# Kernel optimization log

Measured on AMD Instinct MI355X. Metric: run time of the kernel, lower is better.

The kernel has to match this reference:

```python
import jax, jax.numpy as jnp
import numpy as np

DT = 1.0 / 24.0
NEARZERO = 1e-5
LENF = 72
T_STEPS, N_GRID, N_OUT = 1440, 8000, 32

PHY_NAMES = ['parBETA','parFC','parK0','parK1','parK2','parLP','parPERC','parUZL','parTT',
             'parCFMAX','parCFR','parCWH','parBETAET','parC','parRT','parAC','parF0','parFMIN','parALPHA']
PHY_BOUNDS = {'parBETA':(1.0,6.0),'parFC':(50.0,1000.0),'parK0':(0.05,0.9),'parK1':(0.01,0.5),
              'parK2':(0.001,0.2),'parLP':(0.2,1.0),'parPERC':(0.0,10.0),'parUZL':(0.0,100.0),
              'parTT':(-2.5,2.5),'parCFMAX':(0.5,10.0),'parCFR':(0.0,0.1),'parCWH':(0.0,0.2),
              'parBETAET':(0.3,5.0),'parC':(0.0,1.0),'parRT':(0.0,20.0),'parAC':(0.0,2500.0),
              'parF0':(120.0,2880.0),'parFMIN':(0.0,1.0),'parALPHA':(0.5,5.0)}
DISTR_NAMES = ['rout_a','rout_b','rout_tau']
DISTR_BOUNDS = {'rout_a':(0.0,5.0),'rout_b':(0.0,12.0),'rout_tau':(0.0,48.0)}


def _descale(raw, names, bounds):
    # raw in [0,1] -> physical range lb + raw*(ub-lb); each entry is [n_grid]
    return {n: bounds[n][0] + raw[:, i] * (bounds[n][1] - bounds[n][0]) for i, n in enumerate(names)}


def setup_inputs() -> dict:
    key = jax.random.key(0)
    ks = jax.random.split(key, 7)
    u = jax.random.uniform(ks[0], (T_STEPS, N_GRID, 3), dtype=jnp.float32)
    # prcp [0,2) mm/h, tmean [-10,20) C, pet [0,0.3) mm/h
    x_phy = jnp.stack([u[..., 0] * 2.0, u[..., 1] * 30.0 - 10.0, u[..., 2] * 0.3], axis=-1)
    ac_all = jax.random.uniform(ks[1], (N_GRID,), dtype=jnp.float32) * 2000.0        # drainage area km^2
    elev_all = jax.random.uniform(ks[2], (N_GRID,), dtype=jnp.float32) * 3000.0     # elevation m
    outlet_topo = (jax.random.uniform(ks[3], (N_OUT, N_GRID)) < 0.1).astype(jnp.float32)
    areas = jax.random.uniform(ks[4], (N_GRID,), dtype=jnp.float32) * 50.0 + 1.0    # basin area km^2
    params1 = jax.random.uniform(ks[5], (N_GRID, 19), dtype=jnp.float32)            # static phy params
    params2 = jax.random.uniform(ks[6], (N_GRID, 3), dtype=jnp.float32)             # distr routing params
    return {'x_phy': x_phy, 'ac_all': ac_all, 'elev_all': elev_all,
            'outlet_topo': outlet_topo, 'areas': areas, 'params1': params1, 'params2': params2}


def _hbv(x_phy, ac_all, elev_all, outlet_topo, areas, params1, params2):
    p = _descale(params1, PHY_NAMES, PHY_BOUNDS)
    d = _descale(params2, DISTR_NAMES, DISTR_BOUNDS)
    n = x_phy.shape[1]
    init = tuple(jnp.full((n,), 1e-3, x_phy.dtype) for _ in range(5))  # SNOWPACK, MELTWATER, SM, SUZ, SLZ
    # HBV2.0 max hourly infiltration rate, decaying with drainage area (parF0 in mm/day)
    fmax = DT * p['parF0'] * (p['parFMIN'] + (1.0 - p['parFMIN'])
                              * jnp.exp(-(ac_all / (p['parAC'] + 1.0)) ** (1.0 / p['parALPHA'])))

    def step(carry, xt):
        SP, MW, SM, SUZ, SLZ = carry
        P, Tm, PET = xt[:, 0], xt[:, 1], xt[:, 2]
        rain = jnp.where(Tm >= p['parTT'], P, 0.0)
        snow = P - rain
        SP = SP + snow
        melt = jnp.minimum(jnp.maximum(p['parCFMAX'] * DT * (Tm - p['parTT']), 0.0), SP)
        MW = MW + melt; SP = SP - melt
        refr = jnp.minimum(jnp.maximum(p['parCFR'] * p['parCFMAX'] * DT * (p['parTT'] - Tm), 0.0), MW)
        SP = SP + refr; MW = MW - refr
        tosoil = jnp.maximum(MW - p['parCWH'] * SP, 0.0)
        MW = MW - tosoil
        win = rain + tosoil
        infil = jnp.minimum(win, fmax)
        qie = win - infil                                  # infiltration-excess overland flow
        sw = jnp.clip((SM / p['parFC']) ** p['parBETA'], 0.0, 1.0)
        rech = infil * sw
        SM = SM + infil - rech
        excess = jnp.maximum(SM - p['parFC'], 0.0); SM = SM - excess
        cap = jnp.minimum(SLZ, p['parC'] * SLZ * (1.0 - jnp.minimum(SM / p['parFC'], 1.0)))
        SM = SM + cap; SLZ = SLZ - cap                      # capillary rise
        ef = jnp.clip((SM / (p['parLP'] * p['parFC'])) ** p['parBETAET'], 0.0, 1.0)
        et = jnp.minimum(PET * ef, SM)
        SM = jnp.maximum(SM - et, NEARZERO)
        SUZ = SUZ + rech + excess
        perc = jnp.minimum(SUZ, p['parPERC'] * DT); SUZ = SUZ - perc
        q0 = p['parK0'] * DT * jnp.maximum(SUZ - p['parUZL'], 0.0); SUZ = SUZ - q0
        q1 = p['parK1'] * DT * SUZ; SUZ = SUZ - q1
        SLZ = SLZ + perc
        q2 = p['parK2'] * DT * SLZ; SLZ = SLZ - q2
        return (SP, MW, SM, SUZ, SLZ), qie + q0 + q1 + q2

    _, Q = jax.lax.scan(step, init, x_phy)                 # Q: [T, n_grid] grid runoff mm/h

    # Distributed gamma unit hydrograph with per-grid lag (rout_tau + parRT), length LENF hours
    lag = d['rout_tau'] + p['parRT']                       # [n_grid]
    a = jnp.maximum(d['rout_a'], 0.01)
    b = jnp.maximum(d['rout_b'], 0.01)
    tt = jnp.arange(0.5, LENF, 1.0, dtype=x_phy.dtype)     # [LENF]
    s = tt[None, :] - lag[:, None]                          # [n_grid, LENF]
    logw = (a[:, None] - 1.0) * jnp.log(jnp.maximum(s, 1e-6)) - jnp.maximum(s, 1e-6) / b[:, None]
    w = jnp.where(s > 0.0, jnp.exp(logw), 0.0)
    w = w / (jnp.sum(w, axis=1, keepdims=True) + 1e-8)      # normalized per-grid UH [n_grid, LENF]

    # Causal per-grid (depthwise) convolution: routed[t,n] = sum_k w[n,k] * Q[t-k,n]
    lhs = Q.T[None]                                         # [1, n_grid, T]
    rhs = w[:, ::-1][:, None, :]                            # [n_grid, 1, LENF] (flip -> correlation == conv)
    routed = jax.lax.conv_general_dilated(lhs, rhs, (1,), [(LENF - 1, 0)],
                                          feature_group_count=lhs.shape[1])[0].T  # [T, n_grid]
    # Area-weighted aggregation of grid runoff to outlets
    return jnp.einsum('tn,on,n->to', routed, outlet_topo, areas)  # [T, n_out]


def reference(x_phy, ac_all, elev_all, outlet_topo, areas, params1, params2):
    return _hbv(x_phy, ac_all, elev_all, outlet_topo, areas, params1, params2)
```

## Files before the change

### kernel.cpp

```cpp
#include <hip/hip_runtime.h>

#define NG 8000
#define NG3 24000
#define TS 1440
#define NOUT 32
#define LENFT 72
#define DTC (1.0f/24.0f)
#define NEARZEROC 1e-5f

__device__ __forceinline__ float fexp2(float x) {
  float r; asm("v_exp_f32 %0, %1" : "=v"(r) : "v"(x)); return r;
}
__device__ __forceinline__ float flog2(float x) {
  float r; asm("v_log_f32 %0, %1" : "=v"(r) : "v"(x)); return r;
}

typedef const void __attribute__((address_space(1))) gas_void;
typedef void __attribute__((address_space(3)))       las_void;

__global__ __launch_bounds__(256) void precompute_kernel(
    const float* __restrict__ p1, const float* __restrict__ p2,
    const float* __restrict__ ac_all,
    float* __restrict__ Cst,
    float* __restrict__ W)
{
  int n = blockIdx.x * 256 + threadIdx.x;
  if (n >= NG) return;
  const float* r = p1 + n * 19;
  float BETA   = 1.0f   + r[0]  * 5.0f;
  float FC     = 50.0f  + r[1]  * 950.0f;
  float K0     = 0.05f  + r[2]  * 0.85f;
  float K1     = 0.01f  + r[3]  * 0.49f;
  float K2     = 0.001f + r[4]  * 0.199f;
  float LP     = 0.2f   + r[5]  * 0.8f;
  float PERC   =          r[6]  * 10.0f;
  float UZL    =          r[7]  * 100.0f;
  float TT     = -2.5f  + r[8]  * 5.0f;
  float CFMAX  = 0.5f   + r[9]  * 9.5f;
  float CFR    =          r[10] * 0.1f;
  float CWH    =          r[11] * 0.2f;
  float BETAET = 0.3f   + r[12] * 4.7f;
  float Cpar   =          r[13];
  float RT     =          r[14] * 20.0f;
  float AC     =          r[15] * 2500.0f;
  float F0     = 120.0f + r[16] * 2760.0f;
  float FMIN   =          r[17];
  float ALPHA  = 0.5f   + r[18] * 4.5f;

  float ac  = ac_all[n];
  float fmx = DTC * F0 * (FMIN + (1.0f - FMIN) * expf(-powf(ac / (AC + 1.0f), 1.0f / ALPHA)));

  Cst[ 0*NG+n] = TT;            Cst[ 1*NG+n] = CFMAX * DTC;
  Cst[ 2*NG+n] = CFR*CFMAX*DTC; Cst[ 3*NG+n] = CWH;
  Cst[ 4*NG+n] = fmx;           Cst[ 5*NG+n] = 1.0f / FC;
  Cst[ 6*NG+n] = BETA;          Cst[ 7*NG+n] = FC;
  Cst[ 8*NG+n] = Cpar;          Cst[ 9*NG+n] = 1.0f / (LP * FC);
  Cst[10*NG+n] = BETAET;        Cst[11*NG+n] = PERC * DTC;
  Cst[12*NG+n] = K0 * DTC;      Cst[13*NG+n] = UZL;
  Cst[14*NG+n] = K1 * DTC;      Cst[15*NG+n] = K2 * DTC;

  float a   = fmaxf(p2[n*3+0] * 5.0f,  0.01f);
  float b   = fmaxf(p2[n*3+1] * 12.0f, 0.01f);
  float lag = p2[n*3+2] * 48.0f + RT;
  float am1 = a - 1.0f, invb = 1.0f / b;
  float sum = 0.0f;
  for (int k = 0; k < LENFT; k++) {
    float s  = (k + 0.5f) - lag;
    float sm = fmaxf(s, 1e-6f);
    float wv = (s > 0.0f) ? expf(am1 * logf(sm) - sm * invb) : 0.0f;
    sum += wv;
  }
  float inv = 1.0f / (sum + 1e-8f);
  for (int k = 0; k < LENFT; k++) {
    float s  = (k + 0.5f) - lag;
    float sm = fmaxf(s, 1e-6f);
    float wv = (s > 0.0f) ? expf(am1 * logf(sm) - sm * invb) : 0.0f;
    W[k*NG + n] = wv * inv;
  }
}

struct HbvConst {
  float TT, CFMAXDT, CFRDT, CWH, FMX, IFC, BETA, FC, C, ILF, BETAET,
        PERCDT, K0DT, UZL, K1DT, K2DT;
};

__device__ __forceinline__ void load_const(const float* __restrict__ Cst,
                                           int n, HbvConst& c) {
  c.TT    =Cst[ 0*NG+n]; c.CFMAXDT=Cst[ 1*NG+n]; c.CFRDT =Cst[ 2*NG+n];
  c.CWH   =Cst[ 3*NG+n]; c.FMX    =Cst[ 4*NG+n]; c.IFC   =Cst[ 5*NG+n];
  c.BETA  =Cst[ 6*NG+n]; c.FC     =Cst[ 7*NG+n]; c.C     =Cst[ 8*NG+n];
  c.ILF   =Cst[ 9*NG+n]; c.BETAET =Cst[10*NG+n]; c.PERCDT=Cst[11*NG+n];
  c.K0DT  =Cst[12*NG+n]; c.UZL    =Cst[13*NG+n]; c.K1DT  =Cst[14*NG+n];
  c.K2DT  =Cst[15*NG+n];
}

__device__ __forceinline__ float hbv_step(float P, float Tm, float PET,
    const HbvConst& c, float& SP, float& MW, float& SM, float& SUZ, float& SLZ)
{
  bool  w    = Tm >= c.TT;
  float dT   = Tm - c.TT;
  float rain = w ? P : 0.0f;
  SP += P - rain;
  float k  = w ? c.CFMAXDT : c.CFRDT;
  float tr = __builtin_amdgcn_fmed3f(k * dT, -MW, SP);
  MW += tr; SP -= tr;
  float tosoil = fmaxf(MW - c.CWH * SP, 0.0f);
  MW -= tosoil;
  float win   = rain + tosoil;
  float infil = fminf(win, c.FMX);
  float qie   = win - infil;
  float sw    = fminf(fexp2(c.BETA * flog2(SM * c.IFC)), 1.0f);
  float rech  = infil * sw;
  SM += infil - rech;
  float excess = fmaxf(SM - c.FC, 0.0f);
  SM -= excess;
  float u   = fmaxf(1.0f - SM * c.IFC, 0.0f);
  float cap = c.C * SLZ * u;
  SM += cap; SLZ -= cap;
  float ef = fminf(fexp2(c.BETAET * flog2(SM * c.ILF)), 1.0f);
  SM = fmaxf(SM - PET * ef, NEARZEROC);
  SUZ += rech + excess;
  float perc = fminf(SUZ, c.PERCDT);
  SUZ -= perc;
  float q0 = c.K0DT * fmaxf(SUZ - c.UZL, 0.0f);
  SUZ -= q0;
  float q1 = c.K1DT * SUZ;
  SUZ -= q1;
  SLZ += perc;
  float q2 = c.K2DT * SLZ;
  SLZ -= q2;
  return qie + q0 + q1 + q2;
}

#define LOADU8(A, T0)                                                         \
  { _Pragma("unroll")                                                         \
    for (int i_ = 0; i_ < 8; i_++) {                                          \
      const float* b_ = x + (size_t)((T0) + i_) * NG3;                        \
      A[i_] = *reinterpret_cast<const float3*>(b_ + 3 * n);                   \
    } }

__global__ __launch_bounds__(64, 1) void scan_kernel(
    const float* __restrict__ x, const float* __restrict__ Cst,
    float* __restrict__ Q)
{
  int n = blockIdx.x * 64 + threadIdx.x;
  HbvConst c; load_const(Cst, n, c);
  float SP=1e-3f, MW=1e-3f, SM=1e-3f, SUZ=1e-3f, SLZ=1e-3f;

  float3 bufA[8], bufB[8];
  LOADU8(bufA, 0);
  for (int tb = 0; tb < TS; tb += 16) {
    LOADU8(bufB, tb + 8);
    #pragma unroll
    for (int i = 0; i < 8; i++) {
      float* qb = Q + (size_t)(tb + i) * NG;
      qb[n] = hbv_step(bufA[i].x, bufA[i].y, bufA[i].z, c, SP, MW, SM, SUZ, SLZ);
    }
    if (tb + 16 < TS) LOADU8(bufA, tb + 16);
    #pragma unroll
    for (int i = 0; i < 8; i++) {
      float* qb = Q + (size_t)(tb + 8 + i) * NG;
      qb[n] = hbv_step(bufB[i].x, bufB[i].y, bufB[i].z, c, SP, MW, SM, SUZ, SLZ);
    }
  }
}

#define TTILE 48
#define NTILES_T 30
#define NSPLIT 25
#define SUBS 5
#define QROWS (TTILE + 71)
#define NWG (NTILES_T * NSPLIT)

__global__ __launch_bounds__(256, 2) void route_kernel(
    const float* __restrict__ Q, const float* __restrict__ W,
    const float* __restrict__ topo, const float* __restrict__ areas,
    float* __restrict__ Par)
{
  __shared__ float Qs[QROWS][64];
  __shared__ float Ws[LENFT][64];
  __shared__ float Rs[TTILE][68];

  int bid  = blockIdx.x;
  int xcd  = bid & 7, pos = bid >> 3;
  const int q = NWG / 8, r = NWG % 8;
  int wgid = ((xcd < r) ? xcd * (q + 1) : r * (q + 1) + (xcd - r) * q) + pos;
  int tile  = wgid % NTILES_T;
  int split = wgid / NTILES_T;
  int t0    = tile * TTILE;
  int tid   = threadIdx.x;
  int wid   = tid >> 6, lane = tid & 63;

  int nn = tid & 63;
  int tc = wid * 12;
  int oe = tid & 31;
  int te = (tid >> 5) * 6;

  auto stage = [&](int sub) {
    int n0 = (split * SUBS + sub) * 64;
    for (int rr = wid; rr < QROWS; rr += 4) {
      int t = t0 - 71 + rr;
      if (t >= 0)
        __builtin_amdgcn_global_load_lds(
            (gas_void*)(Q + (size_t)t * NG + n0 + lane),
            (las_void*)(&Qs[rr][0]), 4, 0, 0);
      else
        Qs[rr][lane] = 0.0f;
    }
    for (int k = wid; k < LENFT; k += 4)
      __builtin_amdgcn_global_load_lds(
          (gas_void*)(W + (size_t)k * NG + n0 + lane),
          (las_void*)(&Ws[k][0]), 4, 0, 0);
  };

  float acc_out[6] = {0.f, 0.f, 0.f, 0.f, 0.f, 0.f};

  stage(0);
  for (int sub = 0; sub < SUBS; sub++) {
    int n0 = (split * SUBS + sub) * 64;

    float4 Greg[16];
    #pragma unroll
    for (int g4 = 0; g4 < 16; g4++) {
      float4 tv = *reinterpret_cast<const float4*>(&topo[oe * NG + n0 + g4 * 4]);
      float4 av = *reinterpret_cast<const float4*>(&areas[n0 + g4 * 4]);
      Greg[g4] = make_float4(tv.x * av.x, tv.y * av.y, tv.z * av.z, tv.w * av.w);
    }

    __syncthreads();

    float acc[12];
    float qwin[12];
    #pragma unroll
    for (int i = 0; i < 12; i++) { acc[i] = 0.0f; qwin[i] = Qs[tc + i][nn]; }
    #pragma unroll
    for (int kk = 0; kk < LENFT; kk++) {
      float w = Ws[71 - kk][nn];
      #pragma unroll
      for (int i = 0; i < 12; i++) acc[i] += w * qwin[i];
      #pragma unroll
      for (int i = 0; i < 11; i++) qwin[i] = qwin[i + 1];
      if (kk < 71) qwin[11] = Qs[tc + 12 + kk][nn];
    }
    #pragma unroll
    for (int i = 0; i < 12; i++) Rs[tc + i][nn] = acc[i];
    __syncthreads();

    if (sub + 1 < SUBS) stage(sub + 1);

    #pragma unroll
    for (int g4 = 0; g4 < 16; g4++) {
      float4 g = Greg[g4];
      #pragma unroll
      for (int p = 0; p < 6; p++) {
        float4 rv = *reinterpret_cast<const float4*>(&Rs[te + p][g4 * 4]);
        acc_out[p] += rv.x * g.x + rv.y * g.y + rv.z * g.z + rv.w * g.w;
      }
    }
  }

  #pragma unroll
  for (int p = 0; p < 6; p++) {
    int tg = t0 + te + p;
    Par[(split * TS + tg) * NOUT + oe] = acc_out[p];
  }
}

__global__ __launch_bounds__(256) void reduce_kernel(
    const float* __restrict__ Par, float* __restrict__ out)
{
  int i = blockIdx.x * 256 + threadIdx.x;
  if (i < TS * NOUT) {
    float s = 0.0f;
    #pragma unroll
    for (int sp = 0; sp < NSPLIT; sp++) s += Par[sp * (TS * NOUT) + i];
    out[i] = s;
  }
}

extern "C" void kernel_launch(void* const* d_in, const int* in_sizes, int n_in,
                              void* d_out, int out_size, void* d_ws, size_t ws_size,
                              hipStream_t stream)
{
  const float* x_phy  = (const float*)d_in[0];
  const float* ac_all = (const float*)d_in[1];
  const float* topo   = (const float*)d_in[3];
  const float* areas  = (const float*)d_in[4];
  const float* p1     = (const float*)d_in[5];
  const float* p2     = (const float*)d_in[6];
  float* out = (float*)d_out;

  char* ws = (char*)d_ws;
  float* Q   = (float*)(ws);
  float* W   = (float*)(ws + 46080000);
  float* Cst = (float*)(ws + 46080000 + 2304000);
  float* Par = (float*)(ws + 46080000 + 2304000 + 512000);

  hipLaunchKernelGGL(precompute_kernel, dim3(32), dim3(256), 0, stream,
                     p1, p2, ac_all, Cst, W);
  hipLaunchKernelGGL(scan_kernel, dim3(NG / 64), dim3(64), 0, stream,
                     x_phy, Cst, Q);
  hipLaunchKernelGGL(route_kernel, dim3(NWG), dim3(256), 0, stream,
                     Q, W, topo, areas, Par);
  hipLaunchKernelGGL(reduce_kernel, dim3((TS * NOUT + 255) / 256), dim3(256), 0, stream,
                     Par, out);
}
```

Before: 296.6 us.

## Software-pipeline HBV scan by splitting snow and soil stages across time blocks

Splits the per-timestep HBV update into a snow/infiltration stage and a soil/groundwater stage. The snow stage for the next 8-step block now runs interleaved with the soil stage of the current block, with loads rescheduled to match. The aim is more independent instructions in this latency-bound serial scan, which runs with very low occupancy. The cost is more live registers for the staged arrays, plus one redundant snow pass on stale data in the final iteration.

Result: slower. 408.0 us (+37.6%).

```diff
diff --git a/kernel.cpp b/kernel.cpp
--- a/kernel.cpp
+++ b/kernel.cpp
@@ -94,44 +94,6 @@
   c.K2DT  =Cst[15*NG+n];
 }
 
-__device__ __forceinline__ float hbv_step(float P, float Tm, float PET,
-    const HbvConst& c, float& SP, float& MW, float& SM, float& SUZ, float& SLZ)
-{
-  bool  w    = Tm >= c.TT;
-  float dT   = Tm - c.TT;
-  float rain = w ? P : 0.0f;
-  SP += P - rain;
-  float k  = w ? c.CFMAXDT : c.CFRDT;
-  float tr = __builtin_amdgcn_fmed3f(k * dT, -MW, SP);
-  MW += tr; SP -= tr;
-  float tosoil = fmaxf(MW - c.CWH * SP, 0.0f);
-  MW -= tosoil;
-  float win   = rain + tosoil;
-  float infil = fminf(win, c.FMX);
-  float qie   = win - infil;
-  float sw    = fminf(fexp2(c.BETA * flog2(SM * c.IFC)), 1.0f);
-  float rech  = infil * sw;
-  SM += infil - rech;
-  float excess = fmaxf(SM - c.FC, 0.0f);
-  SM -= excess;
-  float u   = fmaxf(1.0f - SM * c.IFC, 0.0f);
-  float cap = c.C * SLZ * u;
-  SM += cap; SLZ -= cap;
-  float ef = fminf(fexp2(c.BETAET * flog2(SM * c.ILF)), 1.0f);
-  SM = fmaxf(SM - PET * ef, NEARZEROC);
-  SUZ += rech + excess;
-  float perc = fminf(SUZ, c.PERCDT);
-  SUZ -= perc;
-  float q0 = c.K0DT * fmaxf(SUZ - c.UZL, 0.0f);
-  SUZ -= q0;
-  float q1 = c.K1DT * SUZ;
-  SUZ -= q1;
-  SLZ += perc;
-  float q2 = c.K2DT * SLZ;
-  SLZ -= q2;
-  return qie + q0 + q1 + q2;
-}
-
 #define LOADU8(A, T0)                                                         \
   { _Pragma("unroll")                                                         \
     for (int i_ = 0; i_ < 8; i_++) {                                          \
@@ -147,21 +109,66 @@
   HbvConst c; load_const(Cst, n, c);
   float SP=1e-3f, MW=1e-3f, SM=1e-3f, SUZ=1e-3f, SLZ=1e-3f;
 
+  auto snow8 = [&](const float3* buf, float* inf, float* qie, float* pet) {
+    #pragma unroll
+    for (int i = 0; i < 8; i++) {
+      float P = buf[i].x, Tm = buf[i].y;
+      bool  w    = Tm >= c.TT;
+      float dT   = Tm - c.TT;
+      float rain = w ? P : 0.0f;
+      SP += P - rain;
+      float k  = w ? c.CFMAXDT : c.CFRDT;
+      float tr = __builtin_amdgcn_fmed3f(k * dT, -MW, SP);
+      MW += tr; SP -= tr;
+      float tos = fmaxf(MW - c.CWH * SP, 0.0f);
+      MW -= tos;
+      float win = rain + tos;
+      float nf  = fminf(win, c.FMX);
+      inf[i] = nf; qie[i] = win - nf; pet[i] = buf[i].z;
+    }
+  };
+  auto soil8 = [&](const float* inf, const float* qie, const float* pet, int tb) {
+    #pragma unroll
+    for (int i = 0; i < 8; i++) {
+      float nf   = inf[i];
+      float sw   = fminf(fexp2(c.BETA * flog2(SM * c.IFC)), 1.0f);
+      float rech = nf * sw;
+      SM += nf - rech;
+      float exc = fmaxf(SM - c.FC, 0.0f);
+      SM -= exc;
+      float u   = fmaxf(1.0f - SM * c.IFC, 0.0f);
+      float cap = c.C * SLZ * u;
+      SM += cap; SLZ -= cap;
+      float ef = fminf(fexp2(c.BETAET * flog2(SM * c.ILF)), 1.0f);
+      SM = fmaxf(SM - pet[i] * ef, NEARZEROC);
+      SUZ += rech + exc;
+      float perc = fminf(SUZ, c.PERCDT);
+      SUZ -= perc;
+      float q0 = c.K0DT * fmaxf(SUZ - c.UZL, 0.0f);
+      SUZ -= q0;
+      float q1 = c.K1DT * SUZ;
+      SUZ -= q1;
+      SLZ += perc;
+      float q2 = c.K2DT * SLZ;
+      SLZ -= q2;
+      (Q + (size_t)(tb + i) * NG)[n] = qie[i] + q0 + q1 + q2;
+    }
+  };
+
   float3 bufA[8], bufB[8];
+  float infA[8], qieA[8], petA[8], infB[8], qieB[8], petB[8];
+
   LOADU8(bufA, 0);
+  snow8(bufA, infA, qieA, petA);
+  LOADU8(bufB, 8);
+
   for (int tb = 0; tb < TS; tb += 16) {
-    LOADU8(bufB, tb + 8);
-    #pragma unroll
-    for (int i = 0; i < 8; i++) {
-      float* qb = Q + (size_t)(tb + i) * NG;
-      qb[n] = hbv_step(bufA[i].x, bufA[i].y, bufA[i].z, c, SP, MW, SM, SUZ, SLZ);
-    }
     if (tb + 16 < TS) LOADU8(bufA, tb + 16);
-    #pragma unroll
-    for (int i = 0; i < 8; i++) {
-      float* qb = Q + (size_t)(tb + 8 + i) * NG;
-      qb[n] = hbv_step(bufB[i].x, bufB[i].y, bufB[i].z, c, SP, MW, SM, SUZ, SLZ);
-    }
+    snow8(bufB, infB, qieB, petB);
+    soil8(infA, qieA, petA, tb);
+    if (tb + 24 < TS) LOADU8(bufB, tb + 24);
+    snow8(bufA, infA, qieA, petA);
+    soil8(infB, qieB, petB, tb + 8);
   }
 }
 
```

## Process two grid cells per thread in HBV scan using packed float2 math

Applied to the files above, without the earlier changes.

The scan kernel now gives each thread two adjacent grid cells and holds the state and constants as 2-wide float vectors, so the compiler can emit packed FP32 ops (v_pk_fma/mul/add) on CDNA. Inputs are loaded as three float2 per timestep and Q is stored as float2, which widens the memory accesses. The trade-off is that the thread count is halved from 8000 to 4000 (63 wavefronts), which lowers latency hiding for the serial recurrence. The exp/log and med3 operations are still scalar.

Result: slower. 399.5 us (+34.7%).

```diff
diff --git a/kernel.cpp b/kernel.cpp
--- a/kernel.cpp
+++ b/kernel.cpp
@@ -1,6 +1,7 @@
 #include <hip/hip_runtime.h>
 
 #define NG 8000
+#define NHALF 4000
 #define NG3 24000
 #define TS 1440
 #define NOUT 32
@@ -17,6 +18,7 @@
 
 typedef const void __attribute__((address_space(1))) gas_void;
 typedef void __attribute__((address_space(3)))       las_void;
+typedef float v2f __attribute__((ext_vector_type(2)));
 
 __global__ __launch_bounds__(256) void precompute_kernel(
     const float* __restrict__ p1, const float* __restrict__ p2,
@@ -79,89 +81,109 @@
   }
 }
 
-struct HbvConst {
-  float TT, CFMAXDT, CFRDT, CWH, FMX, IFC, BETA, FC, C, ILF, BETAET,
-        PERCDT, K0DT, UZL, K1DT, K2DT;
+struct HbvConst2 {
+  v2f TT, CFMAXDT, CFRDT, CWH, FMX, IFC, BETA, FC, C, ILF, BETAET,
+      PERCDT, K0DT, UZL, K1DT, K2DT;
 };
 
-__device__ __forceinline__ void load_const(const float* __restrict__ Cst,
-                                           int n, HbvConst& c) {
-  c.TT    =Cst[ 0*NG+n]; c.CFMAXDT=Cst[ 1*NG+n]; c.CFRDT =Cst[ 2*NG+n];
-  c.CWH   =Cst[ 3*NG+n]; c.FMX    =Cst[ 4*NG+n]; c.IFC   =Cst[ 5*NG+n];
-  c.BETA  =Cst[ 6*NG+n]; c.FC     =Cst[ 7*NG+n]; c.C     =Cst[ 8*NG+n];
-  c.ILF   =Cst[ 9*NG+n]; c.BETAET =Cst[10*NG+n]; c.PERCDT=Cst[11*NG+n];
-  c.K0DT  =Cst[12*NG+n]; c.UZL    =Cst[13*NG+n]; c.K1DT  =Cst[14*NG+n];
-  c.K2DT  =Cst[15*NG+n];
-}
-
-__device__ __forceinline__ float hbv_step(float P, float Tm, float PET,
-    const HbvConst& c, float& SP, float& MW, float& SM, float& SUZ, float& SLZ)
-{
-  bool  w    = Tm >= c.TT;
-  float dT   = Tm - c.TT;
-  float rain = w ? P : 0.0f;
+__device__ __forceinline__ v2f ldc2(const float* __restrict__ Cst, int j, int i2) {
+  return *reinterpret_cast<const v2f*>(Cst + j * NG + i2);
+}
+
+__device__ __forceinline__ v2f hbv_step2p(v2f P, v2f Tm, v2f PET,
+    const HbvConst2& c, v2f& SP, v2f& MW, v2f& SM, v2f& SUZ, v2f& SLZ)
+{
+  const v2f vzero = 0.0f, vone = 1.0f, veps = NEARZEROC;
+  v2f rain, k;
+  rain.x = (Tm.x >= c.TT.x) ? P.x : 0.0f;
+  rain.y = (Tm.y >= c.TT.y) ? P.y : 0.0f;
+  k.x    = (Tm.x >= c.TT.x) ? c.CFMAXDT.x : c.CFRDT.x;
+  k.y    = (Tm.y >= c.TT.y) ? c.CFMAXDT.y : c.CFRDT.y;
+  v2f dT = Tm - c.TT;
   SP += P - rain;
-  float k  = w ? c.CFMAXDT : c.CFRDT;
-  float tr = __builtin_amdgcn_fmed3f(k * dT, -MW, SP);
+  v2f kd = k * dT;
+  v2f tr;
+  tr.x = __builtin_amdgcn_fmed3f(kd.x, -MW.x, SP.x);
+  tr.y = __builtin_amdgcn_fmed3f(kd.y, -MW.y, SP.y);
   MW += tr; SP -= tr;
-  float tosoil = fmaxf(MW - c.CWH * SP, 0.0f);
+  v2f tosoil = __builtin_elementwise_max(MW - c.CWH * SP, vzero);
   MW -= tosoil;
-  float win   = rain + tosoil;
-  float infil = fminf(win, c.FMX);
-  float qie   = win - infil;
-  float sw    = fminf(fexp2(c.BETA * flog2(SM * c.IFC)), 1.0f);
-  float rech  = infil * sw;
+  v2f win   = rain + tosoil;
+  v2f infil = __builtin_elementwise_min(win, c.FMX);
+  v2f qie   = win - infil;
+  v2f lg, sw;
+  lg.x = flog2(SM.x * c.IFC.x);  lg.y = flog2(SM.y * c.IFC.y);
+  sw.x = fexp2(c.BETA.x * lg.x); sw.y = fexp2(c.BETA.y * lg.y);
+  sw = __builtin_elementwise_min(sw, vone);
+  v2f rech = infil * sw;
   SM += infil - rech;
-  float excess = fmaxf(SM - c.FC, 0.0f);
+  v2f excess = __builtin_elementwise_max(SM - c.FC, vzero);
   SM -= excess;
-  float u   = fmaxf(1.0f - SM * c.IFC, 0.0f);
-  float cap = c.C * SLZ * u;
+  v2f u   = __builtin_elementwise_max(vone - SM * c.IFC, vzero);
+  v2f cap = c.C * SLZ * u;
   SM += cap; SLZ -= cap;
-  float ef = fminf(fexp2(c.BETAET * flog2(SM * c.ILF)), 1.0f);
-  SM = fmaxf(SM - PET * ef, NEARZEROC);
+  v2f lg2, ef;
+  lg2.x = flog2(SM.x * c.ILF.x);    lg2.y = flog2(SM.y * c.ILF.y);
+  ef.x  = fexp2(c.BETAET.x * lg2.x); ef.y = fexp2(c.BETAET.y * lg2.y);
+  ef = __builtin_elementwise_min(ef, vone);
+  SM = __builtin_elementwise_max(SM - PET * ef, veps);
   SUZ += rech + excess;
-  float perc = fminf(SUZ, c.PERCDT);
+  v2f perc = __builtin_elementwise_min(SUZ, c.PERCDT);
   SUZ -= perc;
-  float q0 = c.K0DT * fmaxf(SUZ - c.UZL, 0.0f);
+  v2f q0 = c.K0DT * __builtin_elementwise_max(SUZ - c.UZL, vzero);
   SUZ -= q0;
-  float q1 = c.K1DT * SUZ;
+  v2f q1 = c.K1DT * SUZ;
   SUZ -= q1;
   SLZ += perc;
-  float q2 = c.K2DT * SLZ;
+  v2f q2 = c.K2DT * SLZ;
   SLZ -= q2;
   return qie + q0 + q1 + q2;
 }
 
-#define LOADU8(A, T0)                                                         \
+#define LOADP8(A, T0)                                                         \
   { _Pragma("unroll")                                                         \
-    for (int i_ = 0; i_ < 8; i_++) {                                          \
-      const float* b_ = x + (size_t)((T0) + i_) * NG3;                        \
-      A[i_] = *reinterpret_cast<const float3*>(b_ + 3 * n);                   \
+    for (int k_ = 0; k_ < 8; k_++) {                                          \
+      const float* b_ = xp + (size_t)((T0) + k_) * NG3;                       \
+      A[k_][0] = *reinterpret_cast<const v2f*>(b_);                           \
+      A[k_][1] = *reinterpret_cast<const v2f*>(b_ + 2);                       \
+      A[k_][2] = *reinterpret_cast<const v2f*>(b_ + 4);                       \
     } }
+
+#define STEPP(A, k_, t_)                                                      \
+  { v2f P_  = {A[k_][0].x, A[k_][1].y};                                       \
+    v2f Tm_ = {A[k_][0].y, A[k_][2].x};                                       \
+    v2f E_  = {A[k_][1].x, A[k_][2].y};                                       \
+    v2f q_  = hbv_step2p(P_, Tm_, E_, c, SP, MW, SM, SUZ, SLZ);               \
+    *reinterpret_cast<v2f*>(Q + (size_t)(t_) * NG + i2) = q_; }
 
 __global__ __launch_bounds__(64, 1) void scan_kernel(
     const float* __restrict__ x, const float* __restrict__ Cst,
     float* __restrict__ Q)
 {
-  int n = blockIdx.x * 64 + threadIdx.x;
-  HbvConst c; load_const(Cst, n, c);
-  float SP=1e-3f, MW=1e-3f, SM=1e-3f, SUZ=1e-3f, SLZ=1e-3f;
-
-  float3 bufA[8], bufB[8];
-  LOADU8(bufA, 0);
+  int i = blockIdx.x * 64 + threadIdx.x;
+  if (i >= NHALF) return;
+  int i2 = 2 * i;
+
+  HbvConst2 c;
+  c.TT    =ldc2(Cst, 0,i2); c.CFMAXDT=ldc2(Cst, 1,i2); c.CFRDT =ldc2(Cst, 2,i2);
+  c.CWH   =ldc2(Cst, 3,i2); c.FMX    =ldc2(Cst, 4,i2); c.IFC   =ldc2(Cst, 5,i2);
+  c.BETA  =ldc2(Cst, 6,i2); c.FC     =ldc2(Cst, 7,i2); c.C     =ldc2(Cst, 8,i2);
+  c.ILF   =ldc2(Cst, 9,i2); c.BETAET =ldc2(Cst,10,i2); c.PERCDT=ldc2(Cst,11,i2);
+  c.K0DT  =ldc2(Cst,12,i2); c.UZL    =ldc2(Cst,13,i2); c.K1DT  =ldc2(Cst,14,i2);
+  c.K2DT  =ldc2(Cst,15,i2);
+
+  v2f SP = 1e-3f, MW = 1e-3f, SM = 1e-3f, SUZ = 1e-3f, SLZ = 1e-3f;
+  const float* xp = x + (size_t)6 * i;
+
+  v2f bufA[8][3], bufB[8][3];
+  LOADP8(bufA, 0);
   for (int tb = 0; tb < TS; tb += 16) {
-    LOADU8(bufB, tb + 8);
-    #pragma unroll
-    for (int i = 0; i < 8; i++) {
-      float* qb = Q + (size_t)(tb + i) * NG;
-      qb[n] = hbv_step(bufA[i].x, bufA[i].y, bufA[i].z, c, SP, MW, SM, SUZ, SLZ);
-    }
-    if (tb + 16 < TS) LOADU8(bufA, tb + 16);
-    #pragma unroll
-    for (int i = 0; i < 8; i++) {
-      float* qb = Q + (size_t)(tb + 8 + i) * NG;
-      qb[n] = hbv_step(bufB[i].x, bufB[i].y, bufB[i].z, c, SP, MW, SM, SUZ, SLZ);
-    }
+    LOADP8(bufB, tb + 8);
+    #pragma unroll
+    for (int kk = 0; kk < 8; kk++) STEPP(bufA, kk, tb + kk);
+    if (tb + 16 < TS) LOADP8(bufA, tb + 16);
+    #pragma unroll
+    for (int kk = 0; kk < 8; kk++) STEPP(bufB, kk, tb + 8 + kk);
   }
 }
 
@@ -298,7 +320,7 @@
 
   hipLaunchKernelGGL(precompute_kernel, dim3(32), dim3(256), 0, stream,
                      p1, p2, ac_all, Cst, W);
-  hipLaunchKernelGGL(scan_kernel, dim3(NG / 64), dim3(64), 0, stream,
+  hipLaunchKernelGGL(scan_kernel, dim3((NHALF + 63) / 64), dim3(64), 0, stream,
                      x_phy, Cst, Q);
   hipLaunchKernelGGL(route_kernel, dim3(NWG), dim3(256), 0, stream,
                      Q, W, topo, areas, Par);
```

## Fuse scan and routing into a cooperative persistent kernel with progress flags

Applied to the files above, without the earlier changes.

Combines the sequential HBV time scan and the convolution routing into one cooperative launch. 32 high-priority blocks run the scan and bump an atomic progress counter after each 288-step chunk. The remaining persistent blocks spin-wait until the Q rows for their time tile are written, then route, so routing overlaps the scan. The cost is a big change in scan parallelism (256-thread blocks on only 32 CUs instead of 125 small blocks) plus spin-wait overhead. Deadlock is avoided only by the cooperative launch guarantee and a timeout.

Result: slower. 795.8 us (+168.3%).

```diff
diff --git a/kernel.cpp b/kernel.cpp
--- a/kernel.cpp
+++ b/kernel.cpp
@@ -22,8 +22,10 @@
     const float* __restrict__ p1, const float* __restrict__ p2,
     const float* __restrict__ ac_all,
     float* __restrict__ Cst,
-    float* __restrict__ W)
-{
+    float* __restrict__ W,
+    int* __restrict__ prog)
+{
+  if (blockIdx.x == 0 && threadIdx.x == 0) prog[0] = 0;
   int n = blockIdx.x * 256 + threadIdx.x;
   if (n >= NG) return;
   const float* r = p1 + n * 19;
@@ -139,32 +141,6 @@
       A[i_] = *reinterpret_cast<const float3*>(b_ + 3 * n);                   \
     } }
 
-__global__ __launch_bounds__(64, 1) void scan_kernel(
-    const float* __restrict__ x, const float* __restrict__ Cst,
-    float* __restrict__ Q)
-{
-  int n = blockIdx.x * 64 + threadIdx.x;
-  HbvConst c; load_const(Cst, n, c);
-  float SP=1e-3f, MW=1e-3f, SM=1e-3f, SUZ=1e-3f, SLZ=1e-3f;
-
-  float3 bufA[8], bufB[8];
-  LOADU8(bufA, 0);
-  for (int tb = 0; tb < TS; tb += 16) {
-    LOADU8(bufB, tb + 8);
-    #pragma unroll
-    for (int i = 0; i < 8; i++) {
-      float* qb = Q + (size_t)(tb + i) * NG;
-      qb[n] = hbv_step(bufA[i].x, bufA[i].y, bufA[i].z, c, SP, MW, SM, SUZ, SLZ);
-    }
-    if (tb + 16 < TS) LOADU8(bufA, tb + 16);
-    #pragma unroll
-    for (int i = 0; i < 8; i++) {
-      float* qb = Q + (size_t)(tb + 8 + i) * NG;
-      qb[n] = hbv_step(bufB[i].x, bufB[i].y, bufB[i].z, c, SP, MW, SM, SUZ, SLZ);
-    }
-  }
-}
-
 #define TTILE 48
 #define NTILES_T 30
 #define NSPLIT 25
@@ -172,25 +148,14 @@
 #define QROWS (TTILE + 71)
 #define NWG (NTILES_T * NSPLIT)
 
-__global__ __launch_bounds__(256, 2) void route_kernel(
+__device__ __forceinline__ void route_unit(
     const float* __restrict__ Q, const float* __restrict__ W,
     const float* __restrict__ topo, const float* __restrict__ areas,
-    float* __restrict__ Par)
-{
-  __shared__ float Qs[QROWS][64];
-  __shared__ float Ws[LENFT][64];
-  __shared__ float Rs[TTILE][68];
-
-  int bid  = blockIdx.x;
-  int xcd  = bid & 7, pos = bid >> 3;
-  const int q = NWG / 8, r = NWG % 8;
-  int wgid = ((xcd < r) ? xcd * (q + 1) : r * (q + 1) + (xcd - r) * q) + pos;
-  int tile  = wgid % NTILES_T;
-  int split = wgid / NTILES_T;
-  int t0    = tile * TTILE;
-  int tid   = threadIdx.x;
-  int wid   = tid >> 6, lane = tid & 63;
-
+    float* __restrict__ Par, int tile, int split, int tid,
+    float (*Qs)[64], float (*Ws)[64], float (*Rs)[68])
+{
+  int t0  = tile * TTILE;
+  int wid = tid >> 6, lane = tid & 63;
   int nn = tid & 63;
   int tc = wid * 12;
   int oe = tid & 31;
@@ -229,8 +194,7 @@
 
     __syncthreads();
 
-    float acc[12];
-    float qwin[12];
+    float acc[12], qwin[12];
     #pragma unroll
     for (int i = 0; i < 12; i++) { acc[i] = 0.0f; qwin[i] = Qs[tc + i][nn]; }
     #pragma unroll
@@ -266,6 +230,121 @@
   }
 }
 
+#define SCAN_BLKS 32
+#define ROUTE_BLKS 480
+#define CHUNK_T 288
+
+__global__ __launch_bounds__(256, 2) void fused_kernel(
+    const float* __restrict__ x, const float* __restrict__ Cst,
+    float* __restrict__ Q, const float* __restrict__ W,
+    const float* __restrict__ topo, const float* __restrict__ areas,
+    float* __restrict__ Par, int* __restrict__ prog)
+{
+  __shared__ float Qs[QROWS][64];
+  __shared__ float Ws[LENFT][64];
+  __shared__ float Rs[TTILE][68];
+
+  int tid = threadIdx.x;
+
+  if (blockIdx.x < SCAN_BLKS) {
+    __builtin_amdgcn_s_setprio(1);
+    int n = blockIdx.x * 256 + tid;
+    bool act = n < NG;
+    HbvConst c;
+    float SP=1e-3f, MW=1e-3f, SM=1e-3f, SUZ=1e-3f, SLZ=1e-3f;
+    float3 bufA[8], bufB[8];
+    if (act) { load_const(Cst, n, c); LOADU8(bufA, 0); }
+
+    for (int tb = 0; tb < TS; tb += 16) {
+      if (act) {
+        LOADU8(bufB, tb + 8);
+        #pragma unroll
+        for (int i = 0; i < 8; i++) {
+          float* qb = Q + (size_t)(tb + i) * NG;
+          qb[n] = hbv_step(bufA[i].x, bufA[i].y, bufA[i].z, c, SP, MW, SM, SUZ, SLZ);
+        }
+        if (tb + 16 < TS) LOADU8(bufA, tb + 16);
+        #pragma unroll
+        for (int i = 0; i < 8; i++) {
+          float* qb = Q + (size_t)(tb + 8 + i) * NG;
+          qb[n] = hbv_step(bufB[i].x, bufB[i].y, bufB[i].z, c, SP, MW, SM, SUZ, SLZ);
+        }
+      }
+      if (((tb + 16) % CHUNK_T) == 0) {
+        __threadfence();
+        __syncthreads();
+        if (tid == 0) atomicAdd(prog, 1);
+      }
+    }
+  } else {
+    int rb  = blockIdx.x - SCAN_BLKS;
+    int xcd = rb & 7, pos = rb >> 3;
+    int base = xcd * (ROUTE_BLKS / 8) + pos;
+    for (int u = base; u < NWG; u += ROUTE_BLKS) {
+      int tile  = u / NSPLIT;
+      int split = u % NSPLIT;
+      int K    = (48 * tile + 47) / CHUNK_T;
+      int need = SCAN_BLKS * (K + 1);
+      if (tid == 0) {
+        int it = 0;
+        while (__hip_atomic_load(prog, __ATOMIC_ACQUIRE,
+                                 __HIP_MEMORY_SCOPE_AGENT) < need) {
+          __builtin_amdgcn_s_sleep(8);
+          if (++it > 4000000) break;
+        }
+      }
+      __syncthreads();
+      (void)__hip_atomic_load(prog, __ATOMIC_ACQUIRE, __HIP_MEMORY_SCOPE_AGENT);
+      route_unit(Q, W, topo, areas, Par, tile, split, tid, Qs, Ws, Rs);
+      __syncthreads();
+    }
+  }
+}
+
+__global__ __launch_bounds__(64, 1) void scan_kernel(
+    const float* __restrict__ x, const float* __restrict__ Cst,
+    float* __restrict__ Q)
+{
+  int n = blockIdx.x * 64 + threadIdx.x;
+  HbvConst c; load_const(Cst, n, c);
+  float SP=1e-3f, MW=1e-3f, SM=1e-3f, SUZ=1e-3f, SLZ=1e-3f;
+
+  float3 bufA[8], bufB[8];
+  LOADU8(bufA, 0);
+  for (int tb = 0; tb < TS; tb += 16) {
+    LOADU8(bufB, tb + 8);
+    #pragma unroll
+    for (int i = 0; i < 8; i++) {
+      float* qb = Q + (size_t)(tb + i) * NG;
+      qb[n] = hbv_step(bufA[i].x, bufA[i].y, bufA[i].z, c, SP, MW, SM, SUZ, SLZ);
+    }
+    if (tb + 16 < TS) LOADU8(bufA, tb + 16);
+    #pragma unroll
+    for (int i = 0; i < 8; i++) {
+      float* qb = Q + (size_t)(tb + 8 + i) * NG;
+      qb[n] = hbv_step(bufB[i].x, bufB[i].y, bufB[i].z, c, SP, MW, SM, SUZ, SLZ);
+    }
+  }
+}
+
+__global__ __launch_bounds__(256, 2) void route_kernel(
+    const float* __restrict__ Q, const float* __restrict__ W,
+    const float* __restrict__ topo, const float* __restrict__ areas,
+    float* __restrict__ Par)
+{
+  __shared__ float Qs[QROWS][64];
+  __shared__ float Ws[LENFT][64];
+  __shared__ float Rs[TTILE][68];
+
+  int bid  = blockIdx.x;
+  int xcd  = bid & 7, pos = bid >> 3;
+  const int q = NWG / 8, r = NWG % 8;
+  int wgid = ((xcd < r) ? xcd * (q + 1) : r * (q + 1) + (xcd - r) * q) + pos;
+  int tile  = wgid % NTILES_T;
+  int split = wgid / NTILES_T;
+  route_unit(Q, W, topo, areas, Par, tile, split, threadIdx.x, Qs, Ws, Rs);
+}
+
 __global__ __launch_bounds__(256) void reduce_kernel(
     const float* __restrict__ Par, float* __restrict__ out)
 {
@@ -295,13 +374,23 @@
   float* W   = (float*)(ws + 46080000);
   float* Cst = (float*)(ws + 46080000 + 2304000);
   float* Par = (float*)(ws + 46080000 + 2304000 + 512000);
+  int*   prog= (int*)  (ws + 46080000 + 2304000 + 512000 + 4608000);
 
   hipLaunchKernelGGL(precompute_kernel, dim3(32), dim3(256), 0, stream,
-                     p1, p2, ac_all, Cst, W);
-  hipLaunchKernelGGL(scan_kernel, dim3(NG / 64), dim3(64), 0, stream,
-                     x_phy, Cst, Q);
-  hipLaunchKernelGGL(route_kernel, dim3(NWG), dim3(256), 0, stream,
-                     Q, W, topo, areas, Par);
+                     p1, p2, ac_all, Cst, W, prog);
+
+  void* args[] = { (void*)&x_phy, (void*)&Cst, (void*)&Q, (void*)&W,
+                   (void*)&topo, (void*)&areas, (void*)&Par, (void*)&prog };
+  hipError_t e = hipLaunchCooperativeKernel(
+      (const void*)fused_kernel, dim3(SCAN_BLKS + ROUTE_BLKS), dim3(256),
+      args, 0, stream);
+  if (e != hipSuccess) {
+    hipLaunchKernelGGL(scan_kernel, dim3(NG / 64), dim3(64), 0, stream,
+                       x_phy, Cst, Q);
+    hipLaunchKernelGGL(route_kernel, dim3(NWG), dim3(256), 0, stream,
+                       Q, W, topo, areas, Par);
+  }
+
   hipLaunchKernelGGL(reduce_kernel, dim3((TS * NOUT + 255) / 256), dim3(256), 0, stream,
                      Par, out);
 }
```
